# Kernel tuning notes

Hardware: AMD Instinct MI355X
Metric: run time of the kernel (lower is better)

The kernel has to match this reference:

```python
import jax, jax.numpy as jnp
import numpy as np

K = 32            # config.k: active latents per token (batch top-k)
THRESHOLD_LR = 0.01
B, S, F = 8, 256, 16384


def setup_inputs() -> dict:
    key = jax.random.key(0)
    k1, k2 = jax.random.split(key)
    x = jax.random.normal(k1, (B, S, F), dtype=jnp.float32)
    token_mask = jax.random.randint(k2, (B, S), 0, 2, dtype=jnp.int32)
    threshold = jnp.zeros((), dtype=jnp.float32)  # persistent EMA buffer, init 0.0
    return {"x": x, "token_mask": token_mask, "threshold": threshold}


def reference(x, token_mask, threshold):
    # Training path of BatchTopKActivationFunction.forward
    b, s, f = x.shape
    num_tokens = b * s
    k_total = K * num_tokens
    neg_min = jnp.finfo(x.dtype).min
    # mask out tokens: x[~token_mask] = finfo.min (so they never enter top-k)
    xm = jnp.where(token_mask.astype(bool)[:, :, None], x, neg_min)
    flat = xm.reshape(-1)                       # [b*s*f]
    vals, idx = jax.lax.top_k(flat, k_total)    # global top-k over flattened tensor
    # scatter relu'd top-k values back into a zero tensor
    result = jnp.zeros_like(flat).at[idx].set(jax.nn.relu(vals)).reshape(b, s, f)
    # EMA threshold update: min of strictly-positive selected values
    pos = vals > 0
    min_pos = jnp.min(jnp.where(pos, vals, jnp.inf))
    new_threshold = jnp.where(
        jnp.any(pos),
        (1.0 - THRESHOLD_LR) * threshold + THRESHOLD_LR * min_pos,
        threshold,
    )
    return result, new_threshold
```

## Files before the change

kernel.cpp:

```cpp
#include <hip/hip_runtime.h>

#define N_ELEMS   33554432
#define N_TOKENS  2048
#define F4        4096
#define K_TOTAL   65536u
#define NBINS1    4096
#define TLOW      3072

#define C_N1       (NBINS1 + 0)
#define C_NEGMIN   (NBINS1 + 1)
#define C_B1       (NBINS1 + 2)
#define C_KABOVE   (NBINS1 + 3)
#define C_FALLBACK (NBINS1 + 4)
#define LIST1_OFF  (NBINS1 + 16)
#define CAP1       262144u
#define CAP2       4096u

__device__ __forceinline__ unsigned keyOf(float f) {
    unsigned b = __float_as_uint(f);
    return b ^ ((unsigned)((int)b >> 31) | 0x80000000u);
}
__device__ __forceinline__ float valOf(unsigned u) {
    unsigned b = (u & 0x80000000u) ? (u ^ 0x80000000u) : ~u;
    return __uint_as_float(b);
}
__device__ __forceinline__ unsigned umaxu(unsigned a, unsigned b) { return a > b ? a : b; }

__global__ void k_init(unsigned* __restrict__ ws) {
    int t = blockIdx.x * 256 + threadIdx.x;
    if (t < NBINS1 + 16) ws[t] = 0u;
}

__global__ __launch_bounds__(512) void k_hist(const float4* __restrict__ x,
                                              const int* __restrict__ mask,
                                              unsigned* __restrict__ ws) {
    __shared__ unsigned lh[1024];
    const int tok = blockIdx.x;
    if (!mask[tok]) return;
    for (int b = threadIdx.x; b < 1024; b += 512) lh[b] = 0u;
    __syncthreads();
    const float4* xt = x + (size_t)tok * F4;
    for (int j = threadIdx.x; j < F4; j += 512) {
        float4 v = xt[j];
        float fv[4] = {v.x, v.y, v.z, v.w};
        #pragma unroll
        for (int c = 0; c < 4; c++) {
            float f = fv[c];
            if (f >= 2.0f)
                atomicAdd(&lh[(keyOf(f) >> 20) - TLOW], 1u);
        }
    }
    __syncthreads();
    for (int b = threadIdx.x; b < 1024; b += 512) {
        unsigned c = lh[b];
        if (c) atomicAdd(&ws[TLOW + b], c);
    }
}

__global__ void k_scan1(unsigned* __restrict__ ws) {
    __shared__ unsigned sc[1024];
    const int t = threadIdx.x;
    sc[t] = ws[TLOW + t];
    __syncthreads();
    for (int off = 1; off < 1024; off <<= 1) {
        unsigned a = sc[t];
        unsigned b = (t + off < 1024) ? sc[t + off] : 0u;
        __syncthreads();
        sc[t] = a + b;
        __syncthreads();
    }
    unsigned run = sc[t];
    unsigned prev = (t + 1 < 1024) ? sc[t + 1] : 0u;
    if (run >= K_TOTAL && prev < K_TOTAL) {
        ws[C_B1] = (unsigned)(TLOW + t);
        ws[C_KABOVE] = prev;
    }
    if (t == 0 && sc[0] < K_TOTAL) ws[C_FALLBACK] = 1u;
}

__global__ __launch_bounds__(512) void k_hist_fb(const float4* __restrict__ x,
                                                 const int* __restrict__ mask,
                                                 unsigned* __restrict__ ws) {
    if (ws[C_FALLBACK] == 0u) return;
    __shared__ unsigned lh[TLOW];
    __shared__ unsigned s_wmin[8];
    for (int b = threadIdx.x; b < TLOW; b += 512) lh[b] = 0u;
    __syncthreads();
    unsigned negmin = 0u;
    for (int tok = blockIdx.x; tok < N_TOKENS; tok += gridDim.x) {
        if (!mask[tok]) continue;
        const float4* xt = x + (size_t)tok * F4;
        for (int j = threadIdx.x; j < F4; j += 512) {
            float4 v = xt[j];
            float fv[4] = {v.x, v.y, v.z, v.w};
            #pragma unroll
            for (int c = 0; c < 4; c++) {
                float f = fv[c];
                unsigned u = keyOf(f);
                if ((u >> 20) < TLOW) atomicAdd(&lh[u >> 20], 1u);
                if (f > 0.0f) negmin = umaxu(negmin, ~u);
            }
        }
    }
    __syncthreads();
    for (int b = threadIdx.x; b < TLOW; b += 512) {
        unsigned c = lh[b];
        if (c) atomicAdd(&ws[b], c);
    }
    #pragma unroll
    for (int off = 32; off > 0; off >>= 1)
        negmin = umaxu(negmin, __shfl_down(negmin, off, 64));
    int lane = threadIdx.x & 63, w = threadIdx.x >> 6;
    if (lane == 0) s_wmin[w] = negmin;
    __syncthreads();
    if (threadIdx.x == 0) {
        unsigned m = 0u;
        for (int i = 0; i < 8; i++) m = umaxu(m, s_wmin[i]);
        if (m) atomicMax(&ws[C_NEGMIN], m);
    }
}

__global__ void k_scan2(unsigned* __restrict__ ws) {
    if (ws[C_FALLBACK] == 0u) return;
    __shared__ unsigned sc[1024];
    const int t = threadIdx.x;
    const int BPT = NBINS1 / 1024;
    unsigned s = 0u;
    for (int j = 0; j < BPT; j++) s += ws[t * BPT + j];
    sc[t] = s;
    __syncthreads();
    for (int off = 1; off < 1024; off <<= 1) {
        unsigned a = sc[t];
        unsigned b = (t + off < 1024) ? sc[t + off] : 0u;
        __syncthreads();
        sc[t] = a + b;
        __syncthreads();
    }
    unsigned run = (t + 1 < 1024) ? sc[t + 1] : 0u;
    for (int j = BPT - 1; j >= 0; j--) {
        int b = t * BPT + j;
        unsigned prev = run;
        run += ws[b];
        if (run >= K_TOTAL && prev < K_TOTAL) {
            ws[C_B1] = (unsigned)b;
            ws[C_KABOVE] = prev;
        }
    }
    if (t == 0 && sc[0] < K_TOTAL) {
        ws[C_B1] = 0u;
        ws[C_KABOVE] = sc[0] - ws[0];
    }
}

#define P2_BUF 512
__global__ __launch_bounds__(512) void k_pass2(const float4* __restrict__ x,
                                               const int* __restrict__ mask,
                                               unsigned* __restrict__ ws,
                                               float4* __restrict__ out) {
    __shared__ uint2 s_buf[P2_BUF];
    __shared__ unsigned s_cnt, s_base;
    const int tok = blockIdx.x;
    float4* ot = out + (size_t)tok * F4;
    if (!mask[tok]) {
        const float4 z = make_float4(0.f, 0.f, 0.f, 0.f);
        for (int j = threadIdx.x; j < F4; j += 512) ot[j] = z;
        return;
    }
    if (threadIdx.x == 0) s_cnt = 0u;
    __syncthreads();
    const unsigned B1 = ws[C_B1];
    const unsigned loKey = B1 << 20;
    const unsigned hiKey = (B1 + 1u) << 20;
    uint2* list1 = (uint2*)(ws + LIST1_OFF);
    const float4* xt = x + (size_t)tok * F4;
    for (int j = threadIdx.x; j < F4; j += 512) {
        float4 v = xt[j];
        float fv[4] = {v.x, v.y, v.z, v.w};
        float ov[4];
        #pragma unroll
        for (int c = 0; c < 4; c++) {
            float f = fv[c];
            unsigned u = keyOf(f);
            ov[c] = (u >= hiKey && B1 != 4095u) || (B1 == 4095u && (u >> 20) > 4095u)
                        ? fmaxf(f, 0.0f) : 0.0f;
            if ((u >> 20) == B1) {
                unsigned slot = atomicAdd(&s_cnt, 1u);
                uint2 e = make_uint2(u, (unsigned)(tok * (F4 * 4) + j * 4 + c));
                if (slot < P2_BUF) s_buf[slot] = e;
                else {
                    unsigned g = atomicAdd(&ws[C_N1], 1u);
                    if (g < CAP1) list1[g] = e;
                }
            }
        }
        ot[j] = make_float4(ov[0], ov[1], ov[2], ov[3]);
    }
    __syncthreads();
    unsigned cnt = s_cnt > P2_BUF ? P2_BUF : s_cnt;
    if (threadIdx.x == 0) s_base = atomicAdd(&ws[C_N1], cnt);
    __syncthreads();
    for (unsigned j = threadIdx.x; j < cnt; j += 512) {
        unsigned pos = s_base + j;
        if (pos < CAP1) list1[pos] = s_buf[j];
    }
}

__global__ __launch_bounds__(1024) void k_tail(unsigned* __restrict__ ws,
                                               float* __restrict__ out,
                                               const float* __restrict__ thr) {
    __shared__ unsigned h2[256];
    __shared__ uint2 ent[CAP2];
    __shared__ unsigned sMin[1024];
    __shared__ unsigned s_n2;
    __shared__ unsigned s_b2, s_need;
    uint2* list1 = (uint2*)(ws + LIST1_OFF);
    const int t = threadIdx.x;
    unsigned n1 = ws[C_N1]; if (n1 > CAP1) n1 = CAP1;
    if (t < 256) h2[t] = 0u;
    if (t == 0) s_n2 = 0u;
    __syncthreads();
    for (unsigned i = t; i < n1; i += 1024)
        atomicAdd(&h2[(list1[i].x >> 12) & 255u], 1u);
    __syncthreads();
    if (t == 0) {
        unsigned run = ws[C_KABOVE], prev = run;
        int b, found = 0;
        for (b = 255; b >= 0; b--) {
            prev = run;
            run += h2[b];
            if (run >= K_TOTAL) { found = 1; break; }
        }
        if (!found) b = 0;
        s_b2 = (unsigned)b;
        s_need = (K_TOTAL > prev) ? (K_TOTAL - prev) : 1u;
    }
    __syncthreads();
    const unsigned B2 = s_b2, need = s_need;
    for (unsigned i = t; i < n1; i += 1024) {
        uint2 e = list1[i];
        unsigned bb = (e.x >> 12) & 255u;
        if (bb > B2) out[e.y] = fmaxf(valOf(e.x), 0.0f);
        else if (bb == B2) {
            unsigned g = atomicAdd(&s_n2, 1u);
            if (g < CAP2) ent[g] = e;
        }
    }
    __syncthreads();
    unsigned n2 = s_n2 > CAP2 ? CAP2 : s_n2;
    unsigned minSel = 0xFFFFFFFFu;
    for (unsigned i = t; i < n2; i += 1024) {
        uint2 e = ent[i];
        unsigned rank = 0u;
        for (unsigned j = 0; j < n2; j++) {
            uint2 o = ent[j];
            rank += (o.x > e.x || (o.x == e.x && o.y < e.y)) ? 1u : 0u;
        }
        if (rank < need) {
            out[e.y] = fmaxf(valOf(e.x), 0.0f);
            if (e.x < minSel) minSel = e.x;
        }
    }
    sMin[t] = minSel;
    __syncthreads();
    for (int off = 512; off > 0; off >>= 1) {
        if (t < off) sMin[t] = sMin[t] < sMin[t + off] ? sMin[t] : sMin[t + off];
        __syncthreads();
    }
    if (t == 0) {
        float thr_old = thr[0];
        float newt = thr_old;
        unsigned vku = sMin[0];
        if (vku != 0xFFFFFFFFu) {
            float vk = valOf(vku);
            float minpos; int any;
            if (vk > 0.0f) { minpos = vk; any = 1; }
            else {
                unsigned nm = ws[C_NEGMIN];
                any = (nm != 0u);
                minpos = any ? valOf(~nm) : 0.0f;
            }
            if (any) newt = 0.99f * thr_old + 0.01f * minpos;
        }
        out[N_ELEMS] = newt;
    }
}

extern "C" void kernel_launch(void* const* d_in, const int* in_sizes, int n_in,
                              void* d_out, int out_size, void* d_ws, size_t ws_size,
                              hipStream_t stream) {
    const float4* x  = (const float4*)d_in[0];
    const int* mask  = (const int*)d_in[1];
    const float* thr = (const float*)d_in[2];
    float* out       = (float*)d_out;
    unsigned* ws     = (unsigned*)d_ws;

    k_init   <<<(NBINS1 + 16 + 255) / 256, 256, 0, stream>>>(ws);
    k_hist   <<<N_TOKENS, 512, 0, stream>>>(x, mask, ws);
    k_scan1  <<<1, 1024, 0, stream>>>(ws);
    k_hist_fb<<<512, 512, 0, stream>>>(x, mask, ws);
    k_scan2  <<<1, 1024, 0, stream>>>(ws);
    k_pass2  <<<N_TOKENS, 512, 0, stream>>>(x, mask, ws, (float4*)out);
    k_tail   <<<1, 1024, 0, stream>>>(ws, out, thr);
}
```

Baseline: 289.1 us.

## Collect candidates during histogram pass to drop second full read of input

The histogram kernel now also zero-fills the output and appends every value at or above 2.0 (key plus index) to a global candidate list, using finer 4096 bins over that range. A scatter kernel then writes the definite winners and gathers the boundary bin for a rank-based tail, so the second full pass over x (k_pass2) is removed. The old multi-block fallback is replaced by a single-block fallback that only runs when the fast path's assumptions fail. This trades one 128MB read for extra global list writes and a very slow fallback path if it is ever triggered.

```diff
diff --git a/kernel.cpp b/kernel.cpp
--- a/kernel.cpp
+++ b/kernel.cpp
@@ -1,20 +1,27 @@
 #include <hip/hip_runtime.h>
 
-#define N_ELEMS   33554432
-#define N_TOKENS  2048
-#define F4        4096
-#define K_TOTAL   65536u
-#define NBINS1    4096
-#define TLOW      3072
-
-#define C_N1       (NBINS1 + 0)
-#define C_NEGMIN   (NBINS1 + 1)
-#define C_B1       (NBINS1 + 2)
-#define C_KABOVE   (NBINS1 + 3)
-#define C_FALLBACK (NBINS1 + 4)
-#define LIST1_OFF  (NBINS1 + 16)
-#define CAP1       262144u
+#define N_ELEMS  33554432
+#define N4       8388608
+#define N_TOKENS 2048
+#define F4       4096
+#define K_TOTAL  65536u
+#define NBINS    4096
+
+#define C_NG       4096
+#define C_WINTH    4097
+#define C_CANDTH   4098
+#define C_NEED     4099
+#define C_FB       4100
+#define C_N2       4101
+#define N_CTR_END  4160
+
+#define GLIST_OFF  8192u
+#define CAPG       4194304u
+#define LIST2_OFF  (GLIST_OFF + 2u*CAPG)
 #define CAP2       4096u
+#define FB1_OFF    16777216u
+#define CAPF       2097152u
+#define FB2_OFF    (FB1_OFF + 2u*CAPF)
 
 __device__ __forceinline__ unsigned keyOf(float f) {
     unsigned b = __float_as_uint(f);
@@ -28,39 +35,73 @@
 
 __global__ void k_init(unsigned* __restrict__ ws) {
     int t = blockIdx.x * 256 + threadIdx.x;
-    if (t < NBINS1 + 16) ws[t] = 0u;
-}
-
+    if (t < N_CTR_END) ws[t] = 0u;
+}
+
+#define GBUF 1024
 __global__ __launch_bounds__(512) void k_hist(const float4* __restrict__ x,
                                               const int* __restrict__ mask,
-                                              unsigned* __restrict__ ws) {
-    __shared__ unsigned lh[1024];
+                                              unsigned* __restrict__ ws,
+                                              float4* __restrict__ out) {
+    __shared__ unsigned lh[NBINS];
+    __shared__ uint2 sbuf[GBUF];
+    __shared__ unsigned s_cnt, s_base;
     const int tok = blockIdx.x;
-    if (!mask[tok]) return;
-    for (int b = threadIdx.x; b < 1024; b += 512) lh[b] = 0u;
-    __syncthreads();
+    float4* ot = out + (size_t)tok * F4;
+    const float4 z = make_float4(0.f, 0.f, 0.f, 0.f);
+    if (!mask[tok]) {
+        for (int j = threadIdx.x; j < F4; j += 512) ot[j] = z;
+        return;
+    }
+    for (int b = threadIdx.x; b < NBINS; b += 512) lh[b] = 0u;
+    if (threadIdx.x == 0) s_cnt = 0u;
+    __syncthreads();
+    uint2* glist = (uint2*)(ws + GLIST_OFF);
     const float4* xt = x + (size_t)tok * F4;
+    const unsigned baseIdx = (unsigned)tok * 16384u;
     for (int j = threadIdx.x; j < F4; j += 512) {
         float4 v = xt[j];
+        ot[j] = z;
         float fv[4] = {v.x, v.y, v.z, v.w};
         #pragma unroll
         for (int c = 0; c < 4; c++) {
             float f = fv[c];
-            if (f >= 2.0f)
-                atomicAdd(&lh[(keyOf(f) >> 20) - TLOW], 1u);
-        }
-    }
-    __syncthreads();
-    for (int b = threadIdx.x; b < 1024; b += 512) {
+            if (f >= 2.0f) {
+                unsigned u = keyOf(f);
+                unsigned bin = (u - 0xC0000000u) >> 12;
+                if (bin > 4095u) bin = 4095u;
+                atomicAdd(&lh[bin], 1u);
+                unsigned slot = atomicAdd(&s_cnt, 1u);
+                uint2 e = make_uint2(u, baseIdx + (unsigned)j * 4u + (unsigned)c);
+                if (slot < GBUF) sbuf[slot] = e;
+                else { unsigned g = atomicAdd(&ws[C_NG], 1u); if (g < CAPG) glist[g] = e; }
+            }
+        }
+    }
+    __syncthreads();
+    for (int b = threadIdx.x; b < NBINS; b += 512) {
         unsigned c = lh[b];
-        if (c) atomicAdd(&ws[TLOW + b], c);
-    }
-}
-
-__global__ void k_scan1(unsigned* __restrict__ ws) {
+        if (c) atomicAdd(&ws[b], c);
+    }
+    unsigned cnt = s_cnt; if (cnt > GBUF) cnt = GBUF;
+    if (threadIdx.x == 0) s_base = atomicAdd(&ws[C_NG], cnt);
+    __syncthreads();
+    for (unsigned j = threadIdx.x; j < cnt; j += 512) {
+        unsigned p = s_base + j;
+        if (p < CAPG) glist[p] = sbuf[j];
+    }
+}
+
+__global__ __launch_bounds__(1024) void k_scan1(unsigned* __restrict__ ws) {
     __shared__ unsigned sc[1024];
+    __shared__ unsigned sB1, sKA, sFound;
     const int t = threadIdx.x;
-    sc[t] = ws[TLOW + t];
+    unsigned vv[4];
+    unsigned s = 0u;
+    #pragma unroll
+    for (int j = 0; j < 4; ++j) { vv[j] = ws[t * 4 + j]; s += vv[j]; }
+    if (t == 0) sFound = 0u;
+    sc[t] = s;
     __syncthreads();
     for (int off = 1; off < 1024; off <<= 1) {
         unsigned a = sc[t];
@@ -69,217 +110,233 @@
         sc[t] = a + b;
         __syncthreads();
     }
-    unsigned run = sc[t];
-    unsigned prev = (t + 1 < 1024) ? sc[t + 1] : 0u;
-    if (run >= K_TOTAL && prev < K_TOTAL) {
-        ws[C_B1] = (unsigned)(TLOW + t);
-        ws[C_KABOVE] = prev;
-    }
-    if (t == 0 && sc[0] < K_TOTAL) ws[C_FALLBACK] = 1u;
-}
-
-__global__ __launch_bounds__(512) void k_hist_fb(const float4* __restrict__ x,
-                                                 const int* __restrict__ mask,
-                                                 unsigned* __restrict__ ws) {
-    if (ws[C_FALLBACK] == 0u) return;
-    __shared__ unsigned lh[TLOW];
-    __shared__ unsigned s_wmin[8];
-    for (int b = threadIdx.x; b < TLOW; b += 512) lh[b] = 0u;
+    unsigned run = (t < 1023) ? sc[t + 1] : 0u;
+    #pragma unroll
+    for (int j = 3; j >= 0; --j) {
+        unsigned prev = run; run += vv[j];
+        if (run >= K_TOTAL && prev < K_TOTAL) {
+            sB1 = (unsigned)(t * 4 + j); sKA = prev; sFound = 1u;
+        }
+    }
+    __syncthreads();
+    if (t == 0) {
+        unsigned total = sc[0];
+        unsigned ng = ws[C_NG];
+        unsigned fb = (sFound == 0u) || (total < K_TOTAL) || (sB1 == 4095u) || (ng > CAPG);
+        ws[C_FB] = fb ? 1u : 0u;
+        if (!fb) {
+            unsigned candTh = 0xC0000000u + (sB1 << 12);
+            ws[C_CANDTH] = candTh;
+            ws[C_WINTH]  = candTh + 0x1000u;
+            ws[C_NEED]   = K_TOTAL - sKA;
+        }
+    }
+}
+
+__global__ __launch_bounds__(256) void k_scatter(unsigned* __restrict__ ws,
+                                                 float* __restrict__ out) {
+    if (ws[C_FB]) return;
+    const unsigned winTh = ws[C_WINTH], candTh = ws[C_CANDTH];
+    unsigned ng = ws[C_NG]; if (ng > CAPG) ng = CAPG;
+    uint2* glist = (uint2*)(ws + GLIST_OFF);
+    uint2* list2 = (uint2*)(ws + LIST2_OFF);
+    const unsigned stride = gridDim.x * 256;
+    for (unsigned i = blockIdx.x * 256 + threadIdx.x; i < ng; i += stride) {
+        uint2 e = glist[i];
+        if (e.x >= winTh) out[e.y] = valOf(e.x);
+        else if (e.x >= candTh) {
+            unsigned g = atomicAdd(&ws[C_N2], 1u);
+            if (g < CAP2) list2[g] = e;
+        }
+    }
+}
+
+__global__ __launch_bounds__(256) void k_tail(unsigned* __restrict__ ws,
+                                              float* __restrict__ out,
+                                              const float* __restrict__ thr) {
+    if (ws[C_FB]) return;
+    __shared__ uint2 ent[CAP2];
+    __shared__ unsigned sred[256];
+    const int t = threadIdx.x;
+    unsigned rawn2 = ws[C_N2];
+    if (rawn2 > CAP2) { if (t == 0) ws[C_FB] = 1u; return; }
+    const unsigned n2 = rawn2;
+    const unsigned need = ws[C_NEED];
+    uint2* list2 = (uint2*)(ws + LIST2_OFF);
+    for (unsigned i = t; i < n2; i += 256) ent[i] = list2[i];
+    __syncthreads();
+    unsigned minSel = 0xFFFFFFFFu;
+    for (unsigned i = t; i < n2; i += 256) {
+        uint2 e = ent[i];
+        unsigned rank = 0u;
+        for (unsigned j = 0; j < n2; ++j) {
+            uint2 o = ent[j];
+            rank += (o.x > e.x || (o.x == e.x && o.y < e.y)) ? 1u : 0u;
+        }
+        if (rank < need) {
+            out[e.y] = valOf(e.x);
+            if (e.x < minSel) minSel = e.x;
+        }
+    }
+    sred[t] = minSel;
+    __syncthreads();
+    for (int off = 128; off > 0; off >>= 1) {
+        if (t < off) sred[t] = sred[t] < sred[t + off] ? sred[t] : sred[t + off];
+        __syncthreads();
+    }
+    if (t == 0) {
+        out[N_ELEMS] = 0.99f * thr[0] + 0.01f * valOf(sred[0]);
+    }
+}
+
+__global__ __launch_bounds__(1024) void k_fallback(const float4* __restrict__ x,
+                                                   const int* __restrict__ mask,
+                                                   unsigned* __restrict__ ws,
+                                                   float* __restrict__ out,
+                                                   const float* __restrict__ thr) {
+    if (ws[C_FB] == 0u) return;
+    __shared__ unsigned lh[NBINS];
+    __shared__ unsigned sred[1024];
+    __shared__ unsigned sB1, sKA, sMode, sNegmin, sB2, sNeed, sCnt;
+    const int t = threadIdx.x;
+    for (int b = t; b < NBINS; b += 1024) lh[b] = 0u;
     __syncthreads();
     unsigned negmin = 0u;
-    for (int tok = blockIdx.x; tok < N_TOKENS; tok += gridDim.x) {
+    for (int tok = 0; tok < N_TOKENS; ++tok) {
         if (!mask[tok]) continue;
         const float4* xt = x + (size_t)tok * F4;
-        for (int j = threadIdx.x; j < F4; j += 512) {
+        for (int j = t; j < F4; j += 1024) {
             float4 v = xt[j];
             float fv[4] = {v.x, v.y, v.z, v.w};
             #pragma unroll
-            for (int c = 0; c < 4; c++) {
+            for (int c = 0; c < 4; ++c) {
                 float f = fv[c];
                 unsigned u = keyOf(f);
-                if ((u >> 20) < TLOW) atomicAdd(&lh[u >> 20], 1u);
+                atomicAdd(&lh[u >> 20], 1u);
                 if (f > 0.0f) negmin = umaxu(negmin, ~u);
             }
         }
     }
     __syncthreads();
-    for (int b = threadIdx.x; b < TLOW; b += 512) {
-        unsigned c = lh[b];
-        if (c) atomicAdd(&ws[b], c);
-    }
-    #pragma unroll
-    for (int off = 32; off > 0; off >>= 1)
-        negmin = umaxu(negmin, __shfl_down(negmin, off, 64));
-    int lane = threadIdx.x & 63, w = threadIdx.x >> 6;
-    if (lane == 0) s_wmin[w] = negmin;
-    __syncthreads();
-    if (threadIdx.x == 0) {
-        unsigned m = 0u;
-        for (int i = 0; i < 8; i++) m = umaxu(m, s_wmin[i]);
-        if (m) atomicMax(&ws[C_NEGMIN], m);
-    }
-}
-
-__global__ void k_scan2(unsigned* __restrict__ ws) {
-    if (ws[C_FALLBACK] == 0u) return;
-    __shared__ unsigned sc[1024];
-    const int t = threadIdx.x;
-    const int BPT = NBINS1 / 1024;
-    unsigned s = 0u;
-    for (int j = 0; j < BPT; j++) s += ws[t * BPT + j];
-    sc[t] = s;
-    __syncthreads();
-    for (int off = 1; off < 1024; off <<= 1) {
-        unsigned a = sc[t];
-        unsigned b = (t + off < 1024) ? sc[t + off] : 0u;
-        __syncthreads();
-        sc[t] = a + b;
-        __syncthreads();
-    }
-    unsigned run = (t + 1 < 1024) ? sc[t + 1] : 0u;
-    for (int j = BPT - 1; j >= 0; j--) {
-        int b = t * BPT + j;
-        unsigned prev = run;
-        run += ws[b];
-        if (run >= K_TOTAL && prev < K_TOTAL) {
-            ws[C_B1] = (unsigned)b;
-            ws[C_KABOVE] = prev;
-        }
-    }
-    if (t == 0 && sc[0] < K_TOTAL) {
-        ws[C_B1] = 0u;
-        ws[C_KABOVE] = sc[0] - ws[0];
-    }
-}
-
-#define P2_BUF 512
-__global__ __launch_bounds__(512) void k_pass2(const float4* __restrict__ x,
-                                               const int* __restrict__ mask,
-                                               unsigned* __restrict__ ws,
-                                               float4* __restrict__ out) {
-    __shared__ uint2 s_buf[P2_BUF];
-    __shared__ unsigned s_cnt, s_base;
-    const int tok = blockIdx.x;
-    float4* ot = out + (size_t)tok * F4;
-    if (!mask[tok]) {
-        const float4 z = make_float4(0.f, 0.f, 0.f, 0.f);
-        for (int j = threadIdx.x; j < F4; j += 512) ot[j] = z;
+    sred[t] = negmin; __syncthreads();
+    for (int off = 512; off > 0; off >>= 1) {
+        if (t < off) sred[t] = umaxu(sred[t], sred[t + off]);
+        __syncthreads();
+    }
+    if (t == 0) {
+        sNegmin = sred[0];
+        unsigned tot = 0u;
+        for (int b = 0; b < NBINS; ++b) tot += lh[b];
+        if (tot <= K_TOTAL) sMode = 1u;
+        else {
+            sMode = 0u;
+            unsigned run = 0u, prev = 0u; int b1 = 0;
+            for (int b = NBINS - 1; b >= 0; --b) {
+                prev = run; run += lh[b];
+                if (run >= K_TOTAL && prev < K_TOTAL) { b1 = b; break; }
+            }
+            sB1 = (unsigned)b1; sKA = prev;
+        }
+        sCnt = 0u;
+    }
+    __syncthreads();
+    if (sMode == 1u) {
+        for (int tok = 0; tok < N_TOKENS; ++tok) {
+            if (!mask[tok]) continue;
+            const float4* xt = x + (size_t)tok * F4;
+            float* ot = out + (size_t)tok * 16384;
+            for (int j = t; j < F4; j += 1024) {
+                float4 v = xt[j];
+                ot[j * 4 + 0] = fmaxf(v.x, 0.f); ot[j * 4 + 1] = fmaxf(v.y, 0.f);
+                ot[j * 4 + 2] = fmaxf(v.z, 0.f); ot[j * 4 + 3] = fmaxf(v.w, 0.f);
+            }
+        }
+        if (t == 0) {
+            float th = thr[0], newt = th;
+            if (sNegmin) newt = 0.99f * th + 0.01f * valOf(~sNegmin);
+            out[N_ELEMS] = newt;
+        }
         return;
     }
-    if (threadIdx.x == 0) s_cnt = 0u;
-    __syncthreads();
-    const unsigned B1 = ws[C_B1];
-    const unsigned loKey = B1 << 20;
-    const unsigned hiKey = (B1 + 1u) << 20;
-    uint2* list1 = (uint2*)(ws + LIST1_OFF);
-    const float4* xt = x + (size_t)tok * F4;
-    for (int j = threadIdx.x; j < F4; j += 512) {
-        float4 v = xt[j];
-        float fv[4] = {v.x, v.y, v.z, v.w};
-        float ov[4];
-        #pragma unroll
-        for (int c = 0; c < 4; c++) {
-            float f = fv[c];
-            unsigned u = keyOf(f);
-            ov[c] = (u >= hiKey && B1 != 4095u) || (B1 == 4095u && (u >> 20) > 4095u)
-                        ? fmaxf(f, 0.0f) : 0.0f;
-            if ((u >> 20) == B1) {
-                unsigned slot = atomicAdd(&s_cnt, 1u);
-                uint2 e = make_uint2(u, (unsigned)(tok * (F4 * 4) + j * 4 + c));
-                if (slot < P2_BUF) s_buf[slot] = e;
-                else {
-                    unsigned g = atomicAdd(&ws[C_N1], 1u);
-                    if (g < CAP1) list1[g] = e;
+    const unsigned B1c = sB1;
+    uint2* fb1 = (uint2*)(ws + FB1_OFF);
+    for (int tok = 0; tok < N_TOKENS; ++tok) {
+        if (!mask[tok]) continue;
+        const float4* xt = x + (size_t)tok * F4;
+        const unsigned baseIdx = (unsigned)tok * 16384u;
+        for (int j = t; j < F4; j += 1024) {
+            float4 v = xt[j];
+            float fv[4] = {v.x, v.y, v.z, v.w};
+            #pragma unroll
+            for (int c = 0; c < 4; ++c) {
+                float f = fv[c];
+                unsigned u = keyOf(f);
+                unsigned p = u >> 20;
+                unsigned idx = baseIdx + (unsigned)j * 4u + (unsigned)c;
+                if (p > B1c) out[idx] = fmaxf(f, 0.f);
+                else if (p == B1c) {
+                    unsigned g = atomicAdd(&sCnt, 1u);
+                    if (g < CAPF) fb1[g] = make_uint2(u, idx);
                 }
             }
         }
-        ot[j] = make_float4(ov[0], ov[1], ov[2], ov[3]);
-    }
-    __syncthreads();
-    unsigned cnt = s_cnt > P2_BUF ? P2_BUF : s_cnt;
-    if (threadIdx.x == 0) s_base = atomicAdd(&ws[C_N1], cnt);
-    __syncthreads();
-    for (unsigned j = threadIdx.x; j < cnt; j += 512) {
-        unsigned pos = s_base + j;
-        if (pos < CAP1) list1[pos] = s_buf[j];
-    }
-}
-
-__global__ __launch_bounds__(1024) void k_tail(unsigned* __restrict__ ws,
-                                               float* __restrict__ out,
-                                               const float* __restrict__ thr) {
-    __shared__ unsigned h2[256];
-    __shared__ uint2 ent[CAP2];
-    __shared__ unsigned sMin[1024];
-    __shared__ unsigned s_n2;
-    __shared__ unsigned s_b2, s_need;
-    uint2* list1 = (uint2*)(ws + LIST1_OFF);
-    const int t = threadIdx.x;
-    unsigned n1 = ws[C_N1]; if (n1 > CAP1) n1 = CAP1;
-    if (t < 256) h2[t] = 0u;
-    if (t == 0) s_n2 = 0u;
+    }
+    __syncthreads();
+    unsigned n1 = sCnt > CAPF ? CAPF : sCnt;
+    __syncthreads();
+    if (t < 256) lh[t] = 0u;
+    if (t == 0) sCnt = 0u;
     __syncthreads();
     for (unsigned i = t; i < n1; i += 1024)
-        atomicAdd(&h2[(list1[i].x >> 12) & 255u], 1u);
-    __syncthreads();
-    if (t == 0) {
-        unsigned run = ws[C_KABOVE], prev = run;
-        int b, found = 0;
-        for (b = 255; b >= 0; b--) {
-            prev = run;
-            run += h2[b];
-            if (run >= K_TOTAL) { found = 1; break; }
-        }
-        if (!found) b = 0;
-        s_b2 = (unsigned)b;
-        s_need = (K_TOTAL > prev) ? (K_TOTAL - prev) : 1u;
-    }
-    __syncthreads();
-    const unsigned B2 = s_b2, need = s_need;
+        atomicAdd(&lh[(fb1[i].x >> 12) & 255u], 1u);
+    __syncthreads();
+    if (t == 0) {
+        unsigned run = sKA, prev = sKA; int b2 = 0;
+        for (int b = 255; b >= 0; --b) {
+            prev = run; run += lh[b];
+            if (run >= K_TOTAL) { b2 = b; break; }
+        }
+        sB2 = (unsigned)b2; sNeed = K_TOTAL - prev;
+    }
+    __syncthreads();
+    const unsigned B2 = sB2, need = sNeed;
+    uint2* fb2 = (uint2*)(ws + FB2_OFF);
     for (unsigned i = t; i < n1; i += 1024) {
-        uint2 e = list1[i];
+        uint2 e = fb1[i];
         unsigned bb = (e.x >> 12) & 255u;
-        if (bb > B2) out[e.y] = fmaxf(valOf(e.x), 0.0f);
+        if (bb > B2) out[e.y] = fmaxf(valOf(e.x), 0.f);
         else if (bb == B2) {
-            unsigned g = atomicAdd(&s_n2, 1u);
-            if (g < CAP2) ent[g] = e;
-        }
-    }
-    __syncthreads();
-    unsigned n2 = s_n2 > CAP2 ? CAP2 : s_n2;
+            unsigned g = atomicAdd(&sCnt, 1u);
+            if (g < CAPF) fb2[g] = e;
+        }
+    }
+    __syncthreads();
+    unsigned n2 = sCnt > CAPF ? CAPF : sCnt;
     unsigned minSel = 0xFFFFFFFFu;
     for (unsigned i = t; i < n2; i += 1024) {
-        uint2 e = ent[i];
+        uint2 e = fb2[i];
         unsigned rank = 0u;
-        for (unsigned j = 0; j < n2; j++) {
-            uint2 o = ent[j];
+        for (unsigned jj = 0; jj < n2; ++jj) {
+            uint2 o = fb2[jj];
             rank += (o.x > e.x || (o.x == e.x && o.y < e.y)) ? 1u : 0u;
         }
-        if (rank < need) {
-            out[e.y] = fmaxf(valOf(e.x), 0.0f);
-            if (e.x < minSel) minSel = e.x;
-        }
-    }
-    sMin[t] = minSel;
-    __syncthreads();
+        if (rank < need) { out[e.y] = fmaxf(valOf(e.x), 0.f); if (e.x < minSel) minSel = e.x; }
+    }
+    __syncthreads();
+    sred[t] = minSel; __syncthreads();
     for (int off = 512; off > 0; off >>= 1) {
-        if (t < off) sMin[t] = sMin[t] < sMin[t + off] ? sMin[t] : sMin[t + off];
-        __syncthreads();
-    }
-    if (t == 0) {
-        float thr_old = thr[0];
-        float newt = thr_old;
-        unsigned vku = sMin[0];
+        if (t < off) sred[t] = sred[t] < sred[t + off] ? sred[t] : sred[t + off];
+        __syncthreads();
+    }
+    if (t == 0) {
+        float th = thr[0], newt = th;
+        unsigned vku = sred[0];
         if (vku != 0xFFFFFFFFu) {
             float vk = valOf(vku);
             float minpos; int any;
-            if (vk > 0.0f) { minpos = vk; any = 1; }
-            else {
-                unsigned nm = ws[C_NEGMIN];
-                any = (nm != 0u);
-                minpos = any ? valOf(~nm) : 0.0f;
-            }
-            if (any) newt = 0.99f * thr_old + 0.01f * minpos;
+            if (vk > 0.f) { minpos = vk; any = 1; }
+            else { any = (sNegmin != 0u); minpos = any ? valOf(~sNegmin) : 0.f; }
+            if (any) newt = 0.99f * th + 0.01f * minpos;
         }
         out[N_ELEMS] = newt;
     }
@@ -294,11 +351,10 @@
     float* out       = (float*)d_out;
     unsigned* ws     = (unsigned*)d_ws;
 
-    k_init   <<<(NBINS1 + 16 + 255) / 256, 256, 0, stream>>>(ws);
-    k_hist   <<<N_TOKENS, 512, 0, stream>>>(x, mask, ws);
-    k_scan1  <<<1, 1024, 0, stream>>>(ws);
-    k_hist_fb<<<512, 512, 0, stream>>>(x, mask, ws);
-    k_scan2  <<<1, 1024, 0, stream>>>(ws);
-    k_pass2  <<<N_TOKENS, 512, 0, stream>>>(x, mask, ws, (float4*)out);
-    k_tail   <<<1, 1024, 0, stream>>>(ws, out, thr);
-}
+    k_init    <<<17, 256, 0, stream>>>(ws);
+    k_hist    <<<N_TOKENS, 512, 0, stream>>>(x, mask, ws, (float4*)out);
+    k_scan1   <<<1, 1024, 0, stream>>>(ws);
+    k_scatter <<<256, 256, 0, stream>>>(ws, out);
+    k_tail    <<<1, 256, 0, stream>>>(ws, out, thr);
+    k_fallback<<<1, 1024, 0, stream>>>(x, mask, ws, out, thr);
+}
```

New measurement: 272.9 us. -5.6%, faster.
